# Performance work log

Hardware: AMD Instinct MI355X
Metric: run time of the kernel (lower is better)

The kernel has to match this reference:

```python
import jax, jax.numpy as jnp
import numpy as np

N = 64        # SSM state size
L = 262144    # l_max / sequence length


def setup_inputs() -> dict:
    key = jax.random.key(0)
    ks = jax.random.split(key, 8)
    u = jax.random.normal(ks[0], (L,), dtype=jnp.float32)
    # HiPPO-DPLR style eigenvalue init
    Lambda_re = -0.5 * jnp.ones((N,), jnp.float32)
    Lambda_im = jnp.pi * jnp.arange(N, dtype=jnp.float32)
    P_re = jax.random.normal(ks[1], (N,), jnp.float32)
    P_im = jax.random.normal(ks[2], (N,), jnp.float32)
    B_re = jax.random.normal(ks[3], (N,), jnp.float32)
    B_im = jax.random.normal(ks[4], (N,), jnp.float32)
    C_ri = (0.5 ** 0.5) * jax.random.normal(ks[5], (N, 2), jnp.float32)  # C = C_ri[:,0] + i*C_ri[:,1]
    D = jnp.ones((1,), jnp.float32)
    log_step = jax.random.uniform(ks[6], (1,), jnp.float32,
                                  minval=float(np.log(0.001)), maxval=float(np.log(0.1)))
    return {"u": u, "Lambda_re": Lambda_re, "Lambda_im": Lambda_im,
            "P_re": P_re, "P_im": P_im, "B_re": B_re, "B_im": B_im,
            "C_ri": C_ri, "D": D, "log_step": log_step}


def _kernel_DPLR(Lambda, P, Q, B, C, step, l):
    # Evaluate the SSM generating function at the l roots of unity (bilinear discretization)
    Omega = jnp.exp((-2j * jnp.pi) * (jnp.arange(l) / l))          # (L,)
    g = (2.0 / step) * ((1.0 - Omega) / (1.0 + Omega))             # (L,)
    c = 2.0 / (1.0 + Omega)                                        # (L,)
    # Core Cauchy matrix: the single large (L, N) complex intermediate
    recip = 1.0 / (g[:, None] - Lambda[None, :])                   # (L, N)
    # Four Cauchy dot products fused into one thin matmul
    v = jnp.stack([C.conj() * B, C.conj() * P,
                   Q.conj() * B, Q.conj() * P], axis=1)            # (N, 4)
    k = recip @ v                                                  # (L, 4)
    k00, k01, k10, k11 = k[:, 0], k[:, 1], k[:, 2], k[:, 3]
    atRoots = c * (k00 - k01 * (1.0 / (1.0 + k11)) * k10)          # (L,)
    return jnp.fft.ifft(atRoots, l).real                           # (L,) real kernel


def _causal_convolution(u, K):
    l = u.shape[0]
    ud = jnp.fft.rfft(jnp.pad(u, (0, K.shape[0])))
    Kd = jnp.fft.rfft(jnp.pad(K, (0, l)))
    return jnp.fft.irfft(ud * Kd)[:l]


def reference(u, Lambda_re, Lambda_im, P_re, P_im, B_re, B_im, C_ri, D, log_step):
    Lambda = Lambda_re + 1j * Lambda_im
    P = P_re + 1j * P_im
    B = B_re + 1j * B_im
    C = C_ri[:, 0] + 1j * C_ri[:, 1]
    step = jnp.exp(log_step)                                       # (1,)
    K = _kernel_DPLR(Lambda, P, P, B, C, step, u.shape[0])
    return _causal_convolution(u, K) + D * u
```

## Files before the change

### kernel.cpp

```cpp
#include <hip/hip_runtime.h>
#include <math.h>

#define L_LEN  262144
#define N2L    524288
#define NST    64
#define TPB    256
#define PI2F   6.2831853071795864769f
#define PIF    3.1415926535897932385f

__device__ inline float2 cmul(float2 a, float2 b) {
    return make_float2(a.x*b.x - a.y*b.y, a.x*b.y + a.y*b.x);
}

template<int M, int NF>
__device__ float2* lds_fft_r4(float2* b0, float2* b1, float sgn) {
    float2* src = b0; float2* dst = b1;
    int Ns = 1;
    while (Ns * 4 <= M) {
        __syncthreads();
        const int NB = NF * (M / 4);
        for (int bi = threadIdx.x; bi < NB; bi += TPB) {
            int f = bi / (M / 4);
            int j = bi & (M / 4 - 1);
            int r = j & (Ns - 1);
            const float2* s = src + f * M;
            float2 x0 = s[j];
            float2 x1 = s[j +     (M/4)];
            float2 x2 = s[j + 2 * (M/4)];
            float2 x3 = s[j + 3 * (M/4)];
            float ang = sgn * PI2F * ((float)r / (float)(4 * Ns));
            float sn, cs; __sincosf(ang, &sn, &cs);
            float2 w1 = make_float2(cs, sn);
            float2 w2 = cmul(w1, w1);
            float2 w3 = cmul(w2, w1);
            x1 = cmul(x1, w1); x2 = cmul(x2, w2); x3 = cmul(x3, w3);
            float2 t0 = make_float2(x0.x + x2.x, x0.y + x2.y);
            float2 t1 = make_float2(x0.x - x2.x, x0.y - x2.y);
            float2 t2 = make_float2(x1.x + x3.x, x1.y + x3.y);
            float2 t3 = make_float2(x1.x - x3.x, x1.y - x3.y);
            float2* d = dst + f * M + ((j - r) << 2) + r;
            d[0]      = make_float2(t0.x + t2.x, t0.y + t2.y);
            d[Ns]     = make_float2(t1.x - sgn * t3.y, t1.y + sgn * t3.x);
            d[2 * Ns] = make_float2(t0.x - t2.x, t0.y - t2.y);
            d[3 * Ns] = make_float2(t1.x + sgn * t3.y, t1.y - sgn * t3.x);
        }
        float2* t = src; src = dst; dst = t;
        Ns <<= 2;
    }
    if (Ns < M) {
        __syncthreads();
        const int NB = NF * (M / 2);
        for (int bi = threadIdx.x; bi < NB; bi += TPB) {
            int f = bi / (M / 2);
            int j = bi & (M / 2 - 1);
            const float2* s = src + f * M;
            float2 a = s[j];
            float2 b = s[j + M / 2];
            float ang = sgn * PI2F * ((float)j / (float)M);
            float sn, cs; __sincosf(ang, &sn, &cs);
            float2 wb = make_float2(cs * b.x - sn * b.y, cs * b.y + sn * b.x);
            float2* d = dst + f * M + j;
            d[0]     = make_float2(a.x + wb.x, a.y + wb.y);
            d[M / 2] = make_float2(a.x - wb.x, a.y - wb.y);
        }
        float2* t = src; src = dst; dst = t;
    }
    __syncthreads();
    return src;
}

__global__ __launch_bounds__(TPB) void k1_atroots_fft(
    const float* __restrict__ Lre, const float* __restrict__ Lim,
    const float* __restrict__ Pre, const float* __restrict__ Pim,
    const float* __restrict__ Bre, const float* __restrict__ Bim,
    const float* __restrict__ Cri, const float* __restrict__ lstep,
    float2* __restrict__ T1)
{
    __shared__ float2 b0[512], b1[512];
    __shared__ float  sLr[NST], sLi[NST];
    __shared__ float2 sv00[NST], sv01[NST], sv10[NST], sv11[NST];
    int t = threadIdx.x;
    if (t < NST) {
        float lr = Lre[t], li = Lim[t];
        float pr = Pre[t], pi = Pim[t];
        float br = Bre[t], bi = Bim[t];
        float cr = Cri[2*t], ci = Cri[2*t+1];
        sLr[t] = lr; sLi[t] = li;
        sv00[t] = make_float2(cr*br + ci*bi, cr*bi - ci*br);
        sv01[t] = make_float2(cr*pr + ci*pi, cr*pi - ci*pr);
        sv10[t] = make_float2(pr*br + pi*bi, pr*bi - pi*br);
        sv11[t] = make_float2(pr*pr + pi*pi, 0.f);
    }
    __syncthreads();
    int n1 = blockIdx.x;
    float G2 = 2.0f / expf(lstep[0]);
    for (int e = t; e < 512; e += TPB) {
        int j = n1 + (e << 9);
        float h = PIF * ((float)j * (1.0f / (float)L_LEN));
        float sn, cs; __sincosf(h, &sn, &cs);
        float tn = sn * __frcp_rn(cs);
        tn = fminf(fmaxf(tn, -1e7f), 1e7f);
        float gi = G2 * tn;
        float2 k00 = make_float2(0,0), k01 = make_float2(0,0);
        float2 k10 = make_float2(0,0), k11 = make_float2(0,0);
        #pragma unroll
        for (int n = 0; n < NST; ++n) {
            float dx = -sLr[n];
            float dy = gi - sLi[n];
            float iv = __frcp_rn(dx*dx + dy*dy);
            float rx = dx * iv, ry = -dy * iv;
            float2 v;
            v = sv00[n]; k00.x += rx*v.x - ry*v.y; k00.y += rx*v.y + ry*v.x;
            v = sv01[n]; k01.x += rx*v.x - ry*v.y; k01.y += rx*v.y + ry*v.x;
            v = sv10[n]; k10.x += rx*v.x - ry*v.y; k10.y += rx*v.y + ry*v.x;
            v = sv11[n]; k11.x += rx*v.x;          k11.y += ry*v.x;
        }
        float ax = 1.f + k11.x, ay = k11.y;
        float im = 1.f / (ax*ax + ay*ay);
        float tx = k01.x*k10.x - k01.y*k10.y;
        float ty = k01.x*k10.y + k01.y*k10.x;
        float wx = k00.x - (tx*ax + ty*ay) * im;
        float wy = k00.y - (ty*ax - tx*ay) * im;
        b0[e] = make_float2(wx - tn*wy, wy + tn*wx);
    }
    float2* res = lds_fft_r4<512, 1>(b0, b1, +1.f);
    const float invL = 1.0f / (float)L_LEN;
    for (int e = t; e < 512; e += TPB) {
        float ang = PI2F * ((float)(n1 * e) * invL);
        float sn, cs; __sincosf(ang, &sn, &cs);
        T1[(n1 << 9) + e] = cmul(make_float2(cs, sn), res[e]);
    }
}

__global__ __launch_bounds__(TPB) void k2_ifft_pass2_z(
    const float2* __restrict__ T1, const float* __restrict__ u,
    float2* __restrict__ zT)
{
    __shared__ float2 b0[1024], b1[1024];
    int c0 = blockIdx.x << 1;
    for (int i = threadIdx.x; i < 1024; i += TPB) {
        int f = i & 1, e = i >> 1;
        b0[f * 512 + e] = T1[(e << 9) + c0 + f];
    }
    float2* res = lds_fft_r4<512, 2>(b0, b1, +1.f);
    const float invL = 1.0f / (float)L_LEN;
    for (int i = threadIdx.x; i < 1024; i += TPB) {
        int f = i >> 9, k1 = i & 511;
        int c = c0 + f;
        int idx = c + (k1 << 9);
        zT[(c << 9) + k1] = make_float2(u[idx], res[f * 512 + k1].x * invL);
    }
}

__global__ __launch_bounds__(TPB) void k3_fwd_pass1(
    const float2* __restrict__ zT, float2* __restrict__ T2)
{
    __shared__ float2 b0[1024], b1[1024];
    int n1 = blockIdx.x;
    for (int e = threadIdx.x; e < 512; e += TPB)
        b0[e] = zT[(n1 << 9) + e];
    for (int e = 512 + threadIdx.x; e < 1024; e += TPB)
        b0[e] = make_float2(0.f, 0.f);
    float2* res = lds_fft_r4<1024, 1>(b0, b1, -1.f);
    const float inv2L = 1.0f / (float)N2L;
    for (int k2 = threadIdx.x; k2 < 1024; k2 += TPB) {
        float ang = -PI2F * ((float)(n1 * k2) * inv2L);
        float sn, cs; __sincosf(ang, &sn, &cs);
        T2[(n1 << 10) + k2] = cmul(make_float2(cs, sn), res[k2]);
    }
}

__global__ __launch_bounds__(TPB) void k4_fwd_pass2_combine(
    const float2* __restrict__ T2, float2* __restrict__ WT)
{
    __shared__ float2 b0[1024], b1[1024];
    int b  = blockIdx.x;
    int cA = (b == 0) ? 0   : b;
    int cB = (b == 0) ? 512 : 1024 - b;
    for (int i = threadIdx.x; i < 1024; i += TPB) {
        int f = i >> 9, e = i & 511;
        int c = f ? cB : cA;
        b0[f * 512 + e] = T2[(e << 10) + c];
    }
    float2* res = lds_fft_r4<512, 2>(b0, b1, -1.f);
    for (int i = threadIdx.x; i < 1024; i += TPB) {
        int f = i >> 9, k1 = i & 511;
        int c  = f ? cB : cA;
        int mf = (b == 0) ? f : 1 - f;
        int m  = (b == 0 && f == 0) ? ((512 - k1) & 511) : (511 - k1);
        float2 zp = res[f * 512 + k1];
        float2 zq = res[mf * 512 + m];
        float2 U  = make_float2(0.5f * (zp.x + zq.x), 0.5f * (zp.y - zq.y));
        float2 dd = make_float2(zp.x - zq.x, zp.y + zq.y);
        float2 Kf = make_float2(0.5f * dd.y, -0.5f * dd.x);
        WT[(c << 9) + k1] = cmul(U, Kf);
    }
}

__global__ __launch_bounds__(TPB) void k5_inv_pass1(
    const float2* __restrict__ WT, float2* __restrict__ T3)
{
    __shared__ float2 b0[1024], b1[1024];
    int n1 = blockIdx.x;
    for (int e = threadIdx.x; e < 1024; e += TPB) {
        int col = n1 + ((e & 1) << 9);
        b0[e] = WT[(col << 9) + (e >> 1)];
    }
    float2* res = lds_fft_r4<1024, 1>(b0, b1, +1.f);
    const float inv2L = 1.0f / (float)N2L;
    for (int k2 = threadIdx.x; k2 < 1024; k2 += TPB) {
        float ang = PI2F * ((float)(n1 * k2) * inv2L);
        float sn, cs; __sincosf(ang, &sn, &cs);
        T3[(n1 << 10) + k2] = cmul(make_float2(cs, sn), res[k2]);
    }
}

__global__ __launch_bounds__(TPB) void k6_inv_pass2_out(
    const float2* __restrict__ T3, const float* __restrict__ u,
    const float* __restrict__ Dp, float* __restrict__ out)
{
    __shared__ float2 b0[1024], b1[1024];
    int c0 = blockIdx.x << 1;
    for (int i = threadIdx.x; i < 1024; i += TPB) {
        int f = i & 1, e = i >> 1;
        b0[f * 512 + e] = T3[(e << 10) + c0 + f];
    }
    float2* res = lds_fft_r4<512, 2>(b0, b1, +1.f);
    const float inv2L = 1.0f / (float)N2L;
    float D = Dp[0];
    for (int i = threadIdx.x; i < 512; i += TPB) {
        int f = i >> 8, k1 = i & 255;
        int idx = (c0 + f) + (k1 << 10);
        out[idx] = fmaf(D, u[idx], res[f * 512 + k1].x * inv2L);
    }
}

extern "C" void kernel_launch(void* const* d_in, const int* in_sizes, int n_in,
                              void* d_out, int out_size, void* d_ws, size_t ws_size,
                              hipStream_t stream) {
    const float* u    = (const float*)d_in[0];
    const float* Lre  = (const float*)d_in[1];
    const float* Lim  = (const float*)d_in[2];
    const float* Pre  = (const float*)d_in[3];
    const float* Pim  = (const float*)d_in[4];
    const float* Bre  = (const float*)d_in[5];
    const float* Bim  = (const float*)d_in[6];
    const float* Cri  = (const float*)d_in[7];
    const float* Dp   = (const float*)d_in[8];
    const float* lstp = (const float*)d_in[9];
    float* out = (float*)d_out;

    char* ws = (char*)d_ws;
    float2* T1 = (float2*)(ws);
    float2* zT = (float2*)(ws + (2u << 20));
    float2* T2 = (float2*)(ws + (4u << 20));
    float2* WT = (float2*)(ws + (8u << 20));
    float2* T3 = (float2*)(ws);

    k1_atroots_fft      <<<512, TPB, 0, stream>>>(Lre,Lim,Pre,Pim,Bre,Bim,Cri,lstp,T1);
    k2_ifft_pass2_z     <<<256, TPB, 0, stream>>>(T1, u, zT);
    k3_fwd_pass1        <<<512, TPB, 0, stream>>>(zT, T2);
    k4_fwd_pass2_combine<<<512, TPB, 0, stream>>>(T2, WT);
    k5_inv_pass1        <<<512, TPB, 0, stream>>>(WT, T3);
    k6_inv_pass2_out    <<<512, TPB, 0, stream>>>(T3, u, Dp, out);
}
```

Measured before the change: 140.8 us.

## Fuse FFT pipeline into one cooperative kernel with grid syncs

```diff
diff --git a/kernel.cpp b/kernel.cpp
--- a/kernel.cpp
+++ b/kernel.cpp
@@ -1,10 +1,14 @@
 #include <hip/hip_runtime.h>
+#include <hip/hip_cooperative_groups.h>
 #include <math.h>
+
+namespace cg = cooperative_groups;
 
 #define L_LEN  262144
 #define N2L    524288
 #define NST    64
 #define TPB    256
+#define GRID   256
 #define PI2F   6.2831853071795864769f
 #define PIF    3.1415926535897932385f
 
@@ -69,14 +73,14 @@
     return src;
 }
 
-__global__ __launch_bounds__(TPB) void k1_atroots_fft(
+
+__device__ void phase1(int bx, float2* B0, float2* B1,
     const float* __restrict__ Lre, const float* __restrict__ Lim,
     const float* __restrict__ Pre, const float* __restrict__ Pim,
     const float* __restrict__ Bre, const float* __restrict__ Bim,
-    const float* __restrict__ Cri, const float* __restrict__ lstep,
+    const float* __restrict__ Cri, const float* __restrict__ lstp,
     float2* __restrict__ T1)
 {
-    __shared__ float2 b0[512], b1[512];
     __shared__ float  sLr[NST], sLi[NST];
     __shared__ float2 sv00[NST], sv01[NST], sv10[NST], sv11[NST];
     int t = threadIdx.x;
@@ -92,10 +96,11 @@
         sv11[t] = make_float2(pr*pr + pi*pi, 0.f);
     }
     __syncthreads();
-    int n1 = blockIdx.x;
-    float G2 = 2.0f / expf(lstep[0]);
-    for (int e = t; e < 512; e += TPB) {
-        int j = n1 + (e << 9);
+    float G2 = 2.0f / expf(lstp[0]);
+    for (int i = t; i < 1024; i += TPB) {
+        int uu = i >> 9, e = i & 511;
+        int n1 = bx + (uu << 8);
+        int j  = n1 + (e << 9);
         float h = PIF * ((float)j * (1.0f / (float)L_LEN));
         float sn, cs; __sincosf(h, &sn, &cs);
         float tn = sn * __frcp_rn(cs);
@@ -121,118 +126,149 @@
         float ty = k01.x*k10.y + k01.y*k10.x;
         float wx = k00.x - (tx*ax + ty*ay) * im;
         float wy = k00.y - (ty*ax - tx*ay) * im;
-        b0[e] = make_float2(wx - tn*wy, wy + tn*wx);
-    }
-    float2* res = lds_fft_r4<512, 1>(b0, b1, +1.f);
+        B0[i] = make_float2(wx - tn*wy, wy + tn*wx);
+    }
+    float2* r = lds_fft_r4<512, 2>(B0, B1, +1.f);
     const float invL = 1.0f / (float)L_LEN;
-    for (int e = t; e < 512; e += TPB) {
+    for (int i = t; i < 1024; i += TPB) {
+        int uu = i >> 9, e = i & 511;
+        int n1 = bx + (uu << 8);
         float ang = PI2F * ((float)(n1 * e) * invL);
         float sn, cs; __sincosf(ang, &sn, &cs);
-        T1[(n1 << 9) + e] = cmul(make_float2(cs, sn), res[e]);
-    }
-}
-
-__global__ __launch_bounds__(TPB) void k2_ifft_pass2_z(
-    const float2* __restrict__ T1, const float* __restrict__ u,
-    float2* __restrict__ zT)
-{
-    __shared__ float2 b0[1024], b1[1024];
-    int c0 = blockIdx.x << 1;
-    for (int i = threadIdx.x; i < 1024; i += TPB) {
-        int f = i & 1, e = i >> 1;
-        b0[f * 512 + e] = T1[(e << 9) + c0 + f];
-    }
-    float2* res = lds_fft_r4<512, 2>(b0, b1, +1.f);
+        T1[(e << 9) + n1] = cmul(make_float2(cs, sn), r[i]);
+    }
+}
+
+__device__ void phase2(int bx, float2* B0, float2* B1,
+    const float2* __restrict__ T1, const float* __restrict__ uin,
+    float2* __restrict__ T2)
+{
+    int t = threadIdx.x;
+    for (int i = t; i < 1024; i += TPB) {
+        int uu = i >> 9, e = i & 511;
+        B0[i] = T1[((bx + (uu << 8)) << 9) + e];
+    }
+    float2* r = lds_fft_r4<512, 2>(B0, B1, +1.f);
+    float2* o = (r == B0) ? B1 : B0;
     const float invL = 1.0f / (float)L_LEN;
-    for (int i = threadIdx.x; i < 1024; i += TPB) {
+    for (int i = t; i < 1024; i += TPB) {
+        int uu = i >> 9, k1 = i & 511;
+        int c   = bx + (uu << 8);
+        int idx = c + (k1 << 9);
+        o[(uu << 10) + k1]       = make_float2(uin[idx], r[i].x * invL);
+        o[(uu << 10) + 512 + k1] = make_float2(0.f, 0.f);
+    }
+    float2* r2 = lds_fft_r4<1024, 2>(o, r, -1.f);
+    const float inv2L = 1.0f / (float)N2L;
+    for (int i = t; i < 2048; i += TPB) {
+        int uu = i >> 10, k2 = i & 1023;
+        int c = bx + (uu << 8);
+        float ang = -PI2F * ((float)(c * k2) * inv2L);
+        float sn, cs; __sincosf(ang, &sn, &cs);
+        T2[(k2 << 9) + c] = cmul(make_float2(cs, sn), r2[i]);
+    }
+}
+
+__device__ void phase3(int bx, float2* B0, float2* B1,
+    const float2* __restrict__ T2, float2* __restrict__ T3)
+{
+    int t = threadIdx.x;
+    const int q = bx;
+    int cols[4];
+    if (q == 0) { cols[0]=0; cols[1]=512;   cols[2]=256;   cols[3]=768; }
+    else        { cols[0]=q; cols[1]=512+q; cols[2]=512-q; cols[3]=1024-q; }
+    for (int i = t; i < 2048; i += TPB) {
+        int f = i >> 9, e = i & 511;
+        B0[i] = T2[(cols[f] << 9) + e];
+    }
+    float2* r = lds_fft_r4<512, 4>(B0, B1, -1.f);
+    float2* o = (r == B0) ? B1 : B0;
+    for (int i = t; i < 2048; i += TPB) {
         int f = i >> 9, k1 = i & 511;
-        int c = c0 + f;
-        int idx = c + (k1 << 9);
-        zT[(c << 9) + k1] = make_float2(u[idx], res[f * 512 + k1].x * invL);
-    }
-}
-
-__global__ __launch_bounds__(TPB) void k3_fwd_pass1(
-    const float2* __restrict__ zT, float2* __restrict__ T2)
-{
-    __shared__ float2 b0[1024], b1[1024];
-    int n1 = blockIdx.x;
-    for (int e = threadIdx.x; e < 512; e += TPB)
-        b0[e] = zT[(n1 << 9) + e];
-    for (int e = 512 + threadIdx.x; e < 1024; e += TPB)
-        b0[e] = make_float2(0.f, 0.f);
-    float2* res = lds_fft_r4<1024, 1>(b0, b1, -1.f);
+        int mf, m;
+        if (q) { mf = 3 - f;               m = 511 - k1; }
+        else   { mf = (f < 2) ? f : 5 - f; m = (f == 0) ? ((512 - k1) & 511)
+                                                        : (511 - k1); }
+        float2 zp = r[(f  << 9) + k1];
+        float2 zq = r[(mf << 9) + m];
+        float2 U  = make_float2(0.5f*(zp.x + zq.x), 0.5f*(zp.y - zq.y));
+        float2 dd = make_float2(zp.x - zq.x, zp.y + zq.y);
+        float2 Kf = make_float2(0.5f*dd.y, -0.5f*dd.x);
+        o[((f >> 1) << 10) + (k1 << 1) + (f & 1)] = cmul(U, Kf);
+    }
+    float2* r2 = lds_fft_r4<1024, 2>(o, r, +1.f);
     const float inv2L = 1.0f / (float)N2L;
-    for (int k2 = threadIdx.x; k2 < 1024; k2 += TPB) {
-        float ang = -PI2F * ((float)(n1 * k2) * inv2L);
-        float sn, cs; __sincosf(ang, &sn, &cs);
-        T2[(n1 << 10) + k2] = cmul(make_float2(cs, sn), res[k2]);
-    }
-}
-
-__global__ __launch_bounds__(TPB) void k4_fwd_pass2_combine(
-    const float2* __restrict__ T2, float2* __restrict__ WT)
-{
-    __shared__ float2 b0[1024], b1[1024];
-    int b  = blockIdx.x;
-    int cA = (b == 0) ? 0   : b;
-    int cB = (b == 0) ? 512 : 1024 - b;
-    for (int i = threadIdx.x; i < 1024; i += TPB) {
-        int f = i >> 9, e = i & 511;
-        int c = f ? cB : cA;
-        b0[f * 512 + e] = T2[(e << 10) + c];
-    }
-    float2* res = lds_fft_r4<512, 2>(b0, b1, -1.f);
-    for (int i = threadIdx.x; i < 1024; i += TPB) {
-        int f = i >> 9, k1 = i & 511;
-        int c  = f ? cB : cA;
-        int mf = (b == 0) ? f : 1 - f;
-        int m  = (b == 0 && f == 0) ? ((512 - k1) & 511) : (511 - k1);
-        float2 zp = res[f * 512 + k1];
-        float2 zq = res[mf * 512 + m];
-        float2 U  = make_float2(0.5f * (zp.x + zq.x), 0.5f * (zp.y - zq.y));
-        float2 dd = make_float2(zp.x - zq.x, zp.y + zq.y);
-        float2 Kf = make_float2(0.5f * dd.y, -0.5f * dd.x);
-        WT[(c << 9) + k1] = cmul(U, Kf);
-    }
-}
-
-__global__ __launch_bounds__(TPB) void k5_inv_pass1(
-    const float2* __restrict__ WT, float2* __restrict__ T3)
-{
-    __shared__ float2 b0[1024], b1[1024];
-    int n1 = blockIdx.x;
-    for (int e = threadIdx.x; e < 1024; e += TPB) {
-        int col = n1 + ((e & 1) << 9);
-        b0[e] = WT[(col << 9) + (e >> 1)];
-    }
-    float2* res = lds_fft_r4<1024, 1>(b0, b1, +1.f);
-    const float inv2L = 1.0f / (float)N2L;
-    for (int k2 = threadIdx.x; k2 < 1024; k2 += TPB) {
+    for (int i = t; i < 2048; i += TPB) {
+        int s = i >> 10, k2 = i & 1023;
+        int n1 = s ? ((q == 0) ? 256 : 512 - q) : q;
         float ang = PI2F * ((float)(n1 * k2) * inv2L);
         float sn, cs; __sincosf(ang, &sn, &cs);
-        T3[(n1 << 10) + k2] = cmul(make_float2(cs, sn), res[k2]);
-    }
-}
-
-__global__ __launch_bounds__(TPB) void k6_inv_pass2_out(
-    const float2* __restrict__ T3, const float* __restrict__ u,
-    const float* __restrict__ Dp, float* __restrict__ out)
-{
-    __shared__ float2 b0[1024], b1[1024];
-    int c0 = blockIdx.x << 1;
-    for (int i = threadIdx.x; i < 1024; i += TPB) {
-        int f = i & 1, e = i >> 1;
-        b0[f * 512 + e] = T3[(e << 10) + c0 + f];
-    }
-    float2* res = lds_fft_r4<512, 2>(b0, b1, +1.f);
+        T3[(k2 << 9) + n1] = cmul(make_float2(cs, sn), r2[(s << 10) + k2]);
+    }
+}
+
+__device__ void phase4(int bx, float2* B0, float2* B1,
+    const float2* __restrict__ T3, const float* __restrict__ uin,
+    const float* __restrict__ Dp, float* __restrict__ outp)
+{
+    int t = threadIdx.x;
+    int c0 = bx << 2;
+    for (int i = t; i < 2048; i += TPB) {
+        int f = i >> 9, e = i & 511;
+        B0[i] = T3[((c0 + f) << 9) + e];
+    }
+    float2* r = lds_fft_r4<512, 4>(B0, B1, +1.f);
     const float inv2L = 1.0f / (float)N2L;
     float D = Dp[0];
-    for (int i = threadIdx.x; i < 512; i += TPB) {
+    for (int i = t; i < 1024; i += TPB) {
         int f = i >> 8, k1 = i & 255;
         int idx = (c0 + f) + (k1 << 10);
-        out[idx] = fmaf(D, u[idx], res[f * 512 + k1].x * inv2L);
-    }
+        outp[idx] = fmaf(D, uin[idx], r[(f << 9) + k1].x * inv2L);
+    }
+}
+
+__global__ __launch_bounds__(TPB) void s4_mono(
+    const float* u,
+    const float* Lre, const float* Lim, const float* Pre, const float* Pim,
+    const float* Bre, const float* Bim, const float* Cri, const float* Dp,
+    const float* lstp, float* out, float2* T1, float2* T2, float2* T3)
+{
+    cg::grid_group grid = cg::this_grid();
+    __shared__ float2 B0[2048], B1[2048];
+    int bx = blockIdx.x;
+    phase1(bx, B0, B1, Lre, Lim, Pre, Pim, Bre, Bim, Cri, lstp, T1);
+    __threadfence(); grid.sync();
+    phase2(bx, B0, B1, T1, u, T2);
+    __threadfence(); grid.sync();
+    phase3(bx, B0, B1, T2, T3);
+    __threadfence(); grid.sync();
+    phase4(bx, B0, B1, T3, u, Dp, out);
+}
+
+__global__ __launch_bounds__(TPB) void k_p1(
+    const float* Lre, const float* Lim, const float* Pre, const float* Pim,
+    const float* Bre, const float* Bim, const float* Cri, const float* lstp,
+    float2* T1)
+{
+    __shared__ float2 B0[2048], B1[2048];
+    phase1(blockIdx.x, B0, B1, Lre, Lim, Pre, Pim, Bre, Bim, Cri, lstp, T1);
+}
+__global__ __launch_bounds__(TPB) void k_p2(
+    const float2* T1, const float* u, float2* T2)
+{
+    __shared__ float2 B0[2048], B1[2048];
+    phase2(blockIdx.x, B0, B1, T1, u, T2);
+}
+__global__ __launch_bounds__(TPB) void k_p3(const float2* T2, float2* T3)
+{
+    __shared__ float2 B0[2048], B1[2048];
+    phase3(blockIdx.x, B0, B1, T2, T3);
+}
+__global__ __launch_bounds__(TPB) void k_p4(
+    const float2* T3, const float* u, const float* Dp, float* out)
+{
+    __shared__ float2 B0[2048], B1[2048];
+    phase4(blockIdx.x, B0, B1, T3, u, Dp, out);
 }
 
 extern "C" void kernel_launch(void* const* d_in, const int* in_sizes, int n_in,
@@ -252,15 +288,19 @@
 
     char* ws = (char*)d_ws;
     float2* T1 = (float2*)(ws);
-    float2* zT = (float2*)(ws + (2u << 20));
-    float2* T2 = (float2*)(ws + (4u << 20));
-    float2* WT = (float2*)(ws + (8u << 20));
-    float2* T3 = (float2*)(ws);
-
-    k1_atroots_fft      <<<512, TPB, 0, stream>>>(Lre,Lim,Pre,Pim,Bre,Bim,Cri,lstp,T1);
-    k2_ifft_pass2_z     <<<256, TPB, 0, stream>>>(T1, u, zT);
-    k3_fwd_pass1        <<<512, TPB, 0, stream>>>(zT, T2);
-    k4_fwd_pass2_combine<<<512, TPB, 0, stream>>>(T2, WT);
-    k5_inv_pass1        <<<512, TPB, 0, stream>>>(WT, T3);
-    k6_inv_pass2_out    <<<512, TPB, 0, stream>>>(T3, u, Dp, out);
-}
+    float2* T2 = (float2*)(ws + (2u << 20));
+    float2* T3 = (float2*)(ws + (6u << 20));
+
+    void* args[] = { (void*)&u, (void*)&Lre, (void*)&Lim, (void*)&Pre,
+                     (void*)&Pim, (void*)&Bre, (void*)&Bim, (void*)&Cri,
+                     (void*)&Dp, (void*)&lstp, (void*)&out,
+                     (void*)&T1, (void*)&T2, (void*)&T3 };
+    hipError_t err = hipLaunchCooperativeKernel(
+        s4_mono, dim3(GRID), dim3(TPB), args, 0, stream);
+    if (err != hipSuccess) {
+        k_p1<<<GRID, TPB, 0, stream>>>(Lre,Lim,Pre,Pim,Bre,Bim,Cri,lstp,T1);
+        k_p2<<<GRID, TPB, 0, stream>>>(T1, u, T2);
+        k_p3<<<GRID, TPB, 0, stream>>>(T2, T3);
+        k_p4<<<GRID, TPB, 0, stream>>>(T3, u, Dp, out);
+    }
+}
```

Result: slower. 361.8 us (+157.1%).

## Split causal convolution into even/odd length-L FFTs reusing atRoots spectrum

Applied to the files above, without the earlier changes.

```diff
diff --git a/kernel.cpp b/kernel.cpp
--- a/kernel.cpp
+++ b/kernel.cpp
@@ -2,7 +2,6 @@
 #include <math.h>
 
 #define L_LEN  262144
-#define N2L    524288
 #define NST    64
 #define TPB    256
 #define PI2F   6.2831853071795864769f
@@ -69,169 +68,227 @@
     return src;
 }
 
-__global__ __launch_bounds__(TPB) void k1_atroots_fft(
+
+__global__ __launch_bounds__(TPB) void kA(
+    const float* __restrict__ u,
     const float* __restrict__ Lre, const float* __restrict__ Lim,
     const float* __restrict__ Pre, const float* __restrict__ Pim,
     const float* __restrict__ Bre, const float* __restrict__ Bim,
-    const float* __restrict__ Cri, const float* __restrict__ lstep,
-    float2* __restrict__ T1)
-{
-    __shared__ float2 b0[512], b1[512];
+    const float* __restrict__ Cri, const float* __restrict__ lstp,
+    float2* __restrict__ Acm, float2* __restrict__ T_K, float2* __restrict__ T_U)
+{
+    __shared__ float2 b0[1024], b1[1024];
     __shared__ float  sLr[NST], sLi[NST];
     __shared__ float2 sv00[NST], sv01[NST], sv10[NST], sv11[NST];
-    int t = threadIdx.x;
-    if (t < NST) {
-        float lr = Lre[t], li = Lim[t];
-        float pr = Pre[t], pi = Pim[t];
-        float br = Bre[t], bi = Bim[t];
-        float cr = Cri[2*t], ci = Cri[2*t+1];
-        sLr[t] = lr; sLi[t] = li;
-        sv00[t] = make_float2(cr*br + ci*bi, cr*bi - ci*br);
-        sv01[t] = make_float2(cr*pr + ci*pi, cr*pi - ci*pr);
-        sv10[t] = make_float2(pr*br + pi*bi, pr*bi - pi*br);
-        sv11[t] = make_float2(pr*pr + pi*pi, 0.f);
-    }
-    __syncthreads();
-    int n1 = blockIdx.x;
-    float G2 = 2.0f / expf(lstep[0]);
-    for (int e = t; e < 512; e += TPB) {
-        int j = n1 + (e << 9);
-        float h = PIF * ((float)j * (1.0f / (float)L_LEN));
-        float sn, cs; __sincosf(h, &sn, &cs);
-        float tn = sn * __frcp_rn(cs);
-        tn = fminf(fmaxf(tn, -1e7f), 1e7f);
-        float gi = G2 * tn;
-        float2 k00 = make_float2(0,0), k01 = make_float2(0,0);
-        float2 k10 = make_float2(0,0), k11 = make_float2(0,0);
-        #pragma unroll
-        for (int n = 0; n < NST; ++n) {
-            float dx = -sLr[n];
-            float dy = gi - sLi[n];
-            float iv = __frcp_rn(dx*dx + dy*dy);
-            float rx = dx * iv, ry = -dy * iv;
-            float2 v;
-            v = sv00[n]; k00.x += rx*v.x - ry*v.y; k00.y += rx*v.y + ry*v.x;
-            v = sv01[n]; k01.x += rx*v.x - ry*v.y; k01.y += rx*v.y + ry*v.x;
-            v = sv10[n]; k10.x += rx*v.x - ry*v.y; k10.y += rx*v.y + ry*v.x;
-            v = sv11[n]; k11.x += rx*v.x;          k11.y += ry*v.x;
-        }
-        float ax = 1.f + k11.x, ay = k11.y;
-        float im = 1.f / (ax*ax + ay*ay);
-        float tx = k01.x*k10.x - k01.y*k10.y;
-        float ty = k01.x*k10.y + k01.y*k10.x;
-        float wx = k00.x - (tx*ax + ty*ay) * im;
-        float wy = k00.y - (ty*ax - tx*ay) * im;
-        b0[e] = make_float2(wx - tn*wy, wy + tn*wx);
-    }
-    float2* res = lds_fft_r4<512, 1>(b0, b1, +1.f);
+    const int t = threadIdx.x, bx = blockIdx.x;
+    const int c0 = (bx & 255) << 1;
     const float invL = 1.0f / (float)L_LEN;
-    for (int e = t; e < 512; e += TPB) {
-        float ang = PI2F * ((float)(n1 * e) * invL);
-        float sn, cs; __sincosf(ang, &sn, &cs);
-        T1[(n1 << 9) + e] = cmul(make_float2(cs, sn), res[e]);
-    }
-}
-
-__global__ __launch_bounds__(TPB) void k2_ifft_pass2_z(
-    const float2* __restrict__ T1, const float* __restrict__ u,
-    float2* __restrict__ zT)
+    if (bx < 256) {
+        if (t < NST) {
+            float lr = Lre[t], li = Lim[t];
+            float pr = Pre[t], pi = Pim[t];
+            float br = Bre[t], bi = Bim[t];
+            float cr = Cri[2*t], ci = Cri[2*t+1];
+            sLr[t] = lr; sLi[t] = li;
+            sv00[t] = make_float2(cr*br + ci*bi, cr*bi - ci*br);
+            sv01[t] = make_float2(cr*pr + ci*pi, cr*pi - ci*pr);
+            sv10[t] = make_float2(pr*br + pi*bi, pr*bi - pi*br);
+            sv11[t] = make_float2(pr*pr + pi*pi, 0.f);
+        }
+        __syncthreads();
+        float G2 = 2.0f / expf(lstp[0]);
+        for (int i = t; i < 1024; i += TPB) {
+            int f = i >> 9, e = i & 511;
+            int c = c0 + f;
+            int m = c + (e << 9);
+            float h = PIF * ((float)m * invL);
+            float sn, cs; __sincosf(h, &sn, &cs);
+            float tn = sn * __frcp_rn(cs);
+            tn = fminf(fmaxf(tn, -1e7f), 1e7f);
+            float gi = G2 * tn;
+            float2 k00 = make_float2(0,0), k01 = make_float2(0,0);
+            float2 k10 = make_float2(0,0), k11 = make_float2(0,0);
+            #pragma unroll
+            for (int n = 0; n < NST; ++n) {
+                float dx = -sLr[n];
+                float dy = gi - sLi[n];
+                float iv = __frcp_rn(dx*dx + dy*dy);
+                float rx = dx * iv, ry = -dy * iv;
+                float2 v;
+                v = sv00[n]; k00.x += rx*v.x - ry*v.y; k00.y += rx*v.y + ry*v.x;
+                v = sv01[n]; k01.x += rx*v.x - ry*v.y; k01.y += rx*v.y + ry*v.x;
+                v = sv10[n]; k10.x += rx*v.x - ry*v.y; k10.y += rx*v.y + ry*v.x;
+                v = sv11[n]; k11.x += rx*v.x;          k11.y += ry*v.x;
+            }
+            float ax = 1.f + k11.x, ay = k11.y;
+            float im = 1.f / (ax*ax + ay*ay);
+            float tx = k01.x*k10.x - k01.y*k10.y;
+            float ty = k01.x*k10.y + k01.y*k10.x;
+            float wx = k00.x - (tx*ax + ty*ay) * im;
+            float wy = k00.y - (ty*ax - tx*ay) * im;
+            float2 A = make_float2(wx - tn*wy, wy + tn*wx);
+            Acm[(c << 9) + e] = A;
+            b0[i] = A;
+        }
+        float2* r = lds_fft_r4<512, 2>(b0, b1, +1.f);
+        for (int i = t; i < 1024; i += TPB) {
+            int f = i & 1, k = i >> 1;
+            int c = c0 + f;
+            float ang = PI2F * ((float)(c * k) * invL);
+            float sn, cs; __sincosf(ang, &sn, &cs);
+            T_K[(k << 9) + c] = cmul(make_float2(cs, sn), r[(f << 9) + k]);
+        }
+    } else {
+        for (int i = t; i < 1024; i += TPB) {
+            int f = i & 1, e = i >> 1;
+            b0[(f << 9) + e] = make_float2(u[(c0 + f) + (e << 9)], 0.f);
+        }
+        float2* r = lds_fft_r4<512, 2>(b0, b1, -1.f);
+        for (int i = t; i < 1024; i += TPB) {
+            int f = i & 1, k = i >> 1;
+            int c = c0 + f;
+            float ang = -PI2F * ((float)(c * k) * invL);
+            float sn, cs; __sincosf(ang, &sn, &cs);
+            T_U[(k << 9) + c] = cmul(make_float2(cs, sn), r[(f << 9) + k]);
+        }
+    }
+}
+
+__global__ __launch_bounds__(TPB) void kB(
+    const float* __restrict__ u, const float2* __restrict__ T_K,
+    float2* __restrict__ T_Ko, float2* __restrict__ T_Uo)
 {
     __shared__ float2 b0[1024], b1[1024];
-    int c0 = blockIdx.x << 1;
-    for (int i = threadIdx.x; i < 1024; i += TPB) {
-        int f = i & 1, e = i >> 1;
-        b0[f * 512 + e] = T1[(e << 9) + c0 + f];
-    }
-    float2* res = lds_fft_r4<512, 2>(b0, b1, +1.f);
+    const int t = threadIdx.x, bx = blockIdx.x;
+    const int c0 = (bx & 255) << 1;
     const float invL = 1.0f / (float)L_LEN;
-    for (int i = threadIdx.x; i < 1024; i += TPB) {
-        int f = i >> 9, k1 = i & 511;
-        int c = c0 + f;
-        int idx = c + (k1 << 9);
-        zT[(c << 9) + k1] = make_float2(u[idx], res[f * 512 + k1].x * invL);
-    }
-}
-
-__global__ __launch_bounds__(TPB) void k3_fwd_pass1(
-    const float2* __restrict__ zT, float2* __restrict__ T2)
+    if (bx < 256) {
+        for (int i = t; i < 1024; i += TPB)
+            b0[i] = T_K[((c0 + (i >> 9)) << 9) + (i & 511)];
+        float2* r = lds_fft_r4<512, 2>(b0, b1, +1.f);
+        float2* o = (r == b0) ? b1 : b0;
+        for (int i = t; i < 1024; i += TPB) {
+            int f = i >> 9, o1 = i & 511;
+            int n = (c0 + f) + (o1 << 9);
+            float K = r[i].x * invL;
+            float sn, cs; __sincosf(PIF * ((float)n * invL), &sn, &cs);
+            o[i] = make_float2(K * cs, -K * sn);
+        }
+        float2* r2 = lds_fft_r4<512, 2>(o, r, -1.f);
+        for (int i = t; i < 1024; i += TPB) {
+            int f = i & 1, k = i >> 1;
+            int c = c0 + f;
+            float ang = -PI2F * ((float)(c * k) * invL);
+            float sn, cs; __sincosf(ang, &sn, &cs);
+            T_Ko[(k << 9) + c] = cmul(make_float2(cs, sn), r2[(f << 9) + k]);
+        }
+    } else {
+        for (int i = t; i < 1024; i += TPB) {
+            int f = i & 1, e = i >> 1;
+            int n = (c0 + f) + (e << 9);
+            float uv = u[n];
+            float sn, cs; __sincosf(PIF * ((float)n * invL), &sn, &cs);
+            b0[(f << 9) + e] = make_float2(uv * cs, -uv * sn);
+        }
+        float2* r = lds_fft_r4<512, 2>(b0, b1, -1.f);
+        for (int i = t; i < 1024; i += TPB) {
+            int f = i & 1, k = i >> 1;
+            int c = c0 + f;
+            float ang = -PI2F * ((float)(c * k) * invL);
+            float sn, cs; __sincosf(ang, &sn, &cs);
+            T_Uo[(k << 9) + c] = cmul(make_float2(cs, sn), r[(f << 9) + k]);
+        }
+    }
+}
+
+__global__ __launch_bounds__(TPB) void kC(
+    const float2* __restrict__ T_U, const float2* __restrict__ T_Uo,
+    const float2* __restrict__ T_Ko,
+    float2* __restrict__ Ue, float2* __restrict__ Uo, float2* __restrict__ Ko)
 {
     __shared__ float2 b0[1024], b1[1024];
-    int n1 = blockIdx.x;
-    for (int e = threadIdx.x; e < 512; e += TPB)
-        b0[e] = zT[(n1 << 9) + e];
-    for (int e = 512 + threadIdx.x; e < 1024; e += TPB)
-        b0[e] = make_float2(0.f, 0.f);
-    float2* res = lds_fft_r4<1024, 1>(b0, b1, -1.f);
-    const float inv2L = 1.0f / (float)N2L;
-    for (int k2 = threadIdx.x; k2 < 1024; k2 += TPB) {
-        float ang = -PI2F * ((float)(n1 * k2) * inv2L);
-        float sn, cs; __sincosf(ang, &sn, &cs);
-        T2[(n1 << 10) + k2] = cmul(make_float2(cs, sn), res[k2]);
-    }
-}
-
-__global__ __launch_bounds__(TPB) void k4_fwd_pass2_combine(
-    const float2* __restrict__ T2, float2* __restrict__ WT)
+    const int t = threadIdx.x, bx = blockIdx.x;
+    const int s = bx >> 8;
+    const int c0 = (bx & 255) << 1;
+    const float2* Tin = (s == 0) ? T_U : (s == 1) ? T_Uo : T_Ko;
+    float2*       Xo  = (s == 0) ? Ue  : (s == 1) ? Uo   : Ko;
+    for (int i = t; i < 1024; i += TPB)
+        b0[i] = Tin[((c0 + (i >> 9)) << 9) + (i & 511)];
+    float2* r = lds_fft_r4<512, 2>(b0, b1, -1.f);
+    for (int i = t; i < 1024; i += TPB)
+        Xo[((c0 + (i >> 9)) << 9) + (i & 511)] = r[i];
+}
+
+__global__ __launch_bounds__(TPB) void kD(
+    const float2* __restrict__ Ue, const float2* __restrict__ Uo,
+    const float2* __restrict__ Ko, const float2* __restrict__ Acm,
+    float2* __restrict__ T_Ve, float2* __restrict__ T_Vo)
 {
     __shared__ float2 b0[1024], b1[1024];
-    int b  = blockIdx.x;
-    int cA = (b == 0) ? 0   : b;
-    int cB = (b == 0) ? 512 : 1024 - b;
-    for (int i = threadIdx.x; i < 1024; i += TPB) {
-        int f = i >> 9, e = i & 511;
-        int c = f ? cB : cA;
-        b0[f * 512 + e] = T2[(e << 10) + c];
-    }
-    float2* res = lds_fft_r4<512, 2>(b0, b1, -1.f);
-    for (int i = threadIdx.x; i < 1024; i += TPB) {
-        int f = i >> 9, k1 = i & 511;
-        int c  = f ? cB : cA;
-        int mf = (b == 0) ? f : 1 - f;
-        int m  = (b == 0 && f == 0) ? ((512 - k1) & 511) : (511 - k1);
-        float2 zp = res[f * 512 + k1];
-        float2 zq = res[mf * 512 + m];
-        float2 U  = make_float2(0.5f * (zp.x + zq.x), 0.5f * (zp.y - zq.y));
-        float2 dd = make_float2(zp.x - zq.x, zp.y + zq.y);
-        float2 Kf = make_float2(0.5f * dd.y, -0.5f * dd.x);
-        WT[(c << 9) + k1] = cmul(U, Kf);
-    }
-}
-
-__global__ __launch_bounds__(TPB) void k5_inv_pass1(
-    const float2* __restrict__ WT, float2* __restrict__ T3)
-{
-    __shared__ float2 b0[1024], b1[1024];
-    int n1 = blockIdx.x;
-    for (int e = threadIdx.x; e < 1024; e += TPB) {
-        int col = n1 + ((e & 1) << 9);
-        b0[e] = WT[(col << 9) + (e >> 1)];
-    }
-    float2* res = lds_fft_r4<1024, 1>(b0, b1, +1.f);
-    const float inv2L = 1.0f / (float)N2L;
-    for (int k2 = threadIdx.x; k2 < 1024; k2 += TPB) {
-        float ang = PI2F * ((float)(n1 * k2) * inv2L);
-        float sn, cs; __sincosf(ang, &sn, &cs);
-        T3[(n1 << 10) + k2] = cmul(make_float2(cs, sn), res[k2]);
-    }
-}
-
-__global__ __launch_bounds__(TPB) void k6_inv_pass2_out(
-    const float2* __restrict__ T3, const float* __restrict__ u,
-    const float* __restrict__ Dp, float* __restrict__ out)
-{
-    __shared__ float2 b0[1024], b1[1024];
-    int c0 = blockIdx.x << 1;
-    for (int i = threadIdx.x; i < 1024; i += TPB) {
-        int f = i & 1, e = i >> 1;
-        b0[f * 512 + e] = T3[(e << 10) + c0 + f];
-    }
-    float2* res = lds_fft_r4<512, 2>(b0, b1, +1.f);
-    const float inv2L = 1.0f / (float)N2L;
-    float D = Dp[0];
-    for (int i = threadIdx.x; i < 512; i += TPB) {
-        int f = i >> 8, k1 = i & 255;
-        int idx = (c0 + f) + (k1 << 10);
-        out[idx] = fmaf(D, u[idx], res[f * 512 + k1].x * inv2L);
+    const int t = threadIdx.x, bx = blockIdx.x;
+    const int c0 = (bx & 255) << 1;
+    const float invL = 1.0f / (float)L_LEN;
+    if (bx < 256) {
+        for (int i = t; i < 1024; i += TPB) {
+            int f = i >> 9, k1 = i & 511;
+            int c = c0 + f;
+            float2 ue = Ue[(c << 9) + k1];
+            float2 a  = Acm[(c << 9) + k1];
+            int cm = (512 - c) & 511;
+            int km = (c == 0) ? ((512 - k1) & 511) : (511 - k1);
+            float2 am = Acm[(cm << 9) + km];
+            float2 ah = make_float2(0.5f * (a.x + am.x), 0.5f * (a.y - am.y));
+            b0[i] = cmul(ue, ah);
+        }
+        float2* r = lds_fft_r4<512, 2>(b0, b1, +1.f);
+        for (int i = t; i < 1024; i += TPB) {
+            int f = i & 1, k = i >> 1;
+            int c = c0 + f;
+            float ang = PI2F * ((float)(c * k) * invL);
+            float sn, cs; __sincosf(ang, &sn, &cs);
+            T_Ve[(k << 9) + c] = cmul(make_float2(cs, sn), r[(f << 9) + k]);
+        }
+    } else {
+        for (int i = t; i < 1024; i += TPB) {
+            int f = i >> 9, k1 = i & 511;
+            int c = c0 + f;
+            b0[i] = cmul(Uo[(c << 9) + k1], Ko[(c << 9) + k1]);
+        }
+        float2* r = lds_fft_r4<512, 2>(b0, b1, +1.f);
+        for (int i = t; i < 1024; i += TPB) {
+            int f = i & 1, k = i >> 1;
+            int c = c0 + f;
+            float ang = PI2F * ((float)(c * k) * invL);
+            float sn, cs; __sincosf(ang, &sn, &cs);
+            T_Vo[(k << 9) + c] = cmul(make_float2(cs, sn), r[(f << 9) + k]);
+        }
+    }
+}
+
+__global__ __launch_bounds__(TPB) void kE(
+    const float2* __restrict__ T_Ve, const float2* __restrict__ T_Vo,
+    const float* __restrict__ u, const float* __restrict__ Dp,
+    float* __restrict__ out)
+{
+    __shared__ float2 b0[2048], b1[2048];
+    const int t = threadIdx.x, bx = blockIdx.x;
+    const int c0 = bx << 1;
+    const float invL = 1.0f / (float)L_LEN;
+    for (int i = t; i < 1024; i += TPB) {
+        int f = i >> 9, m1 = i & 511;
+        b0[i]        = T_Ve[((c0 + f) << 9) + m1];
+        b0[i + 1024] = T_Vo[((c0 + f) << 9) + m1];
+    }
+    float2* r = lds_fft_r4<512, 4>(b0, b1, +1.f);
+    const float sc = 0.5f * invL;
+    const float D = Dp[0];
+    for (int i = t; i < 1024; i += TPB) {
+        int f = i & 1, o1 = i >> 1;
+        int n = (c0 + f) + (o1 << 9);
+        float sn, cs; __sincosf(PIF * ((float)n * invL), &sn, &cs);
+        float2 yE = r[(f << 9) + o1];
+        float2 yO = r[((f + 2) << 9) + o1];
+        out[n] = fmaf(D, u[n], (yE.x + cs * yO.x - sn * yO.y) * sc);
     }
 }
 
@@ -251,16 +308,20 @@
     float* out = (float*)d_out;
 
     char* ws = (char*)d_ws;
-    float2* T1 = (float2*)(ws);
-    float2* zT = (float2*)(ws + (2u << 20));
-    float2* T2 = (float2*)(ws + (4u << 20));
-    float2* WT = (float2*)(ws + (8u << 20));
-    float2* T3 = (float2*)(ws);
-
-    k1_atroots_fft      <<<512, TPB, 0, stream>>>(Lre,Lim,Pre,Pim,Bre,Bim,Cri,lstp,T1);
-    k2_ifft_pass2_z     <<<256, TPB, 0, stream>>>(T1, u, zT);
-    k3_fwd_pass1        <<<512, TPB, 0, stream>>>(zT, T2);
-    k4_fwd_pass2_combine<<<512, TPB, 0, stream>>>(T2, WT);
-    k5_inv_pass1        <<<512, TPB, 0, stream>>>(WT, T3);
-    k6_inv_pass2_out    <<<512, TPB, 0, stream>>>(T3, u, Dp, out);
-}
+    float2* Acm  = (float2*)(ws);
+    float2* T_K  = (float2*)(ws + ( 2u << 20));
+    float2* T_U  = (float2*)(ws + ( 4u << 20));
+    float2* T_Ko = (float2*)(ws + ( 6u << 20));
+    float2* T_Uo = (float2*)(ws + ( 8u << 20));
+    float2* Ue   = (float2*)(ws + (10u << 20));
+    float2* Uo   = (float2*)(ws + (12u << 20));
+    float2* Ko   = (float2*)(ws + (14u << 20));
+    float2* T_Ve = (float2*)(ws + (16u << 20));
+    float2* T_Vo = (float2*)(ws + (18u << 20));
+
+    kA<<<512, TPB, 0, stream>>>(u, Lre,Lim,Pre,Pim,Bre,Bim,Cri,lstp, Acm, T_K, T_U);
+    kB<<<512, TPB, 0, stream>>>(u, T_K, T_Ko, T_Uo);
+    kC<<<768, TPB, 0, stream>>>(T_U, T_Uo, T_Ko, Ue, Uo, Ko);
+    kD<<<512, TPB, 0, stream>>>(Ue, Uo, Ko, Acm, T_Ve, T_Vo);
+    kE<<<256, TPB, 0, stream>>>(T_Ve, T_Vo, u, Dp, out);
+}
```

New measurement: 135.2 us. 1.04x faster.
